# Performance work log

Measured on AMD Instinct MI355X. Metric: run time of the kernel, lower is better.

## Reference

```python
import jax, jax.numpy as jnp
import numpy as np

DEPTH = 6
DIM = 512
HEADS = 8
DH = DIM // HEADS            # 64 head dim
NB = int(DH * np.log(DH))    # 266 FAVOR+ random features (lucidrains default)
FF = 4 * DIM
OUT = 32
B, N = 4, 8192
EPS = 1e-4


def _orthogonal_gaussian(rng, m, d):
    # Blockwise QR orthogonal random matrix with chi-distributed row norms (scaling=0)
    blocks, full = [], m // d
    for _ in range(full):
        q, _ = np.linalg.qr(rng.standard_normal((d, d)))
        blocks.append(q.T)
    rem = m - full * d
    if rem > 0:
        q, _ = np.linalg.qr(rng.standard_normal((d, d)))
        blocks.append(q.T[:rem])
    mat = np.concatenate(blocks, 0)
    mult = np.linalg.norm(rng.standard_normal((m, d)), axis=1)
    return (mult[:, None] * mat).astype(np.float32)


def setup_inputs() -> dict:
    key = jax.random.key(0)
    ks = jax.random.split(key, 16)
    rng = np.random.default_rng(0)
    s = 0.02
    inp = {
        "src": jax.random.normal(ks[0], (B, N, DIM), jnp.float32),
        "proj": jnp.asarray(np.stack([_orthogonal_gaussian(rng, NB, DH) for _ in range(DEPTH)])),
        "ln1_g": jnp.ones((DEPTH, DIM), jnp.float32),
        "ln1_b": jnp.zeros((DEPTH, DIM), jnp.float32),
        "Wq": jax.random.normal(ks[1], (DEPTH, DIM, DIM), jnp.float32) * s,
        "Wk": jax.random.normal(ks[2], (DEPTH, DIM, DIM), jnp.float32) * s,
        "Wv": jax.random.normal(ks[3], (DEPTH, DIM, DIM), jnp.float32) * s,
        "Wo": jax.random.normal(ks[4], (DEPTH, DIM, DIM), jnp.float32) * s,
        "bo": jnp.zeros((DEPTH, DIM), jnp.float32),
        "ln2_g": jnp.ones((DEPTH, DIM), jnp.float32),
        "ln2_b": jnp.zeros((DEPTH, DIM), jnp.float32),
        "W1": jax.random.normal(ks[5], (DEPTH, DIM, FF), jnp.float32) * s,
        "b1": jnp.zeros((DEPTH, FF), jnp.float32),
        "W2": jax.random.normal(ks[6], (DEPTH, FF, DIM), jnp.float32) * s,
        "b2": jnp.zeros((DEPTH, DIM), jnp.float32),
        "fc_w": jax.random.uniform(ks[7], (DIM, OUT), jnp.float32, -0.1, 0.1),
        "fc_b": jnp.zeros((OUT,), jnp.float32),
    }
    return inp


def _layer_norm(x, g, b):
    mu = jnp.mean(x, -1, keepdims=True)
    var = jnp.var(x, -1, keepdims=True)
    return (x - mu) * jax.lax.rsqrt(var + 1e-5) * g + b


def _softmax_kernel(x, proj, is_query):
    # x: [b,h,n,dh], proj: [m,dh] -> positive random features [b,h,n,m]
    dn = DH ** -0.25
    ratio = NB ** -0.5
    xp = jnp.einsum('bhnd,md->bhnm', x * dn, proj)
    diag = (0.5 * jnp.sum(jnp.square(x), -1) * dn * dn)[..., None]
    if is_query:
        mx = jax.lax.stop_gradient(jnp.max(xp, axis=-1, keepdims=True))
    else:
        mx = jax.lax.stop_gradient(jnp.max(xp))
    return ratio * (jnp.exp(xp - diag - mx) + EPS)


def _performer_forward(src, proj, ln1_g, ln1_b, Wq, Wk, Wv, Wo, bo,
                       ln2_g, ln2_b, W1, b1, W2, b2, fc_w, fc_b):
    b, n, _ = src.shape
    x = src
    for i in range(DEPTH):
        h = _layer_norm(x, ln1_g[i], ln1_b[i])
        q = jnp.einsum('bnd,de->bne', h, Wq[i]).reshape(b, n, HEADS, DH).swapaxes(1, 2)
        k = jnp.einsum('bnd,de->bne', h, Wk[i]).reshape(b, n, HEADS, DH).swapaxes(1, 2)
        v = jnp.einsum('bnd,de->bne', h, Wv[i]).reshape(b, n, HEADS, DH).swapaxes(1, 2)
        qp = _softmax_kernel(q, proj[i], True)    # [b,h,n,m]
        kp = _softmax_kernel(k, proj[i], False)
        k_sum = jnp.sum(kp, axis=2)               # [b,h,m]
        d_inv = 1.0 / jnp.einsum('bhnm,bhm->bhn', qp, k_sum)
        ctx = jnp.einsum('bhnm,bhnd->bhmd', kp, v)  # linear-time attention context
        o = jnp.einsum('bhnm,bhmd,bhn->bhnd', qp, ctx, d_inv)
        o = o.swapaxes(1, 2).reshape(b, n, DIM)
        x = x + jnp.einsum('bnd,de->bne', o, Wo[i]) + bo[i]
        h2 = _layer_norm(x, ln2_g[i], ln2_b[i])
        ff = jax.nn.gelu(jnp.einsum('bnd,df->bnf', h2, W1[i]) + b1[i])
        x = x + jnp.einsum('bnf,fd->bnd', ff, W2[i]) + b2[i]
    return jnp.einsum('bnd,do->bno', x, fc_w) + fc_b


def reference(src, proj, ln1_g, ln1_b, Wq, Wk, Wv, Wo, bo,
              ln2_g, ln2_b, W1, b1, W2, b2, fc_w, fc_b):
    return _performer_forward(src, proj, ln1_g, ln1_b, Wq, Wk, Wv, Wo, bo,
                              ln2_g, ln2_b, W1, b1, W2, b2, fc_w, fc_b)
```

## Files before the change

### kernel.cpp

```cpp
#include <hip/hip_runtime.h>
#include <math.h>

#define DIMX 512
#define NHEADS 8
#define DHE 64
#define NB 266
#define MP 288
#define MT 18
#define KPT_LD 136
#define CTXT_LD 296
#define NSTRIP 32
#define FFD 2048
#define OUTD 32
#define SEQ 8192
#define NTOK 32768
#define NLAYER 6
#define PSEQ 16384

#define DN_F 0.35355339059327373f
#define RATIO_F 0.06131393f
#define EPS_F 1e-4f

typedef unsigned short ushort_t;
typedef __attribute__((ext_vector_type(8))) short short8;
typedef __attribute__((ext_vector_type(4))) float floatx4;

__device__ __forceinline__ float tanh_fast(float x) {
    float e = __expf(2.0f * x);
    return 1.0f - 2.0f / (e + 1.0f);
}

__device__ __forceinline__ float gelu_f(float x) {
    float x3 = x * x * x;
    return 0.5f * x * (1.0f + tanh_fast(0.7978845608028654f * (x + 0.044715f * x3)));
}

__device__ __forceinline__ ushort_t f2bf(float f) {
    unsigned int u = __float_as_uint(f);
    unsigned int r = (u + 0x7fffu + ((u >> 16) & 1u)) >> 16;
    return (ushort_t)r;
}

__device__ __forceinline__ float bf2f(ushort_t u) {
    return __uint_as_float(((unsigned int)u) << 16);
}

__device__ __forceinline__ unsigned int fkey(float f) {
    unsigned int u = __float_as_uint(f);
    return (u & 0x80000000u) ? ~u : (u | 0x80000000u);
}
__device__ __forceinline__ float funkey(unsigned int k) {
    unsigned int u = (k & 0x80000000u) ? (k & 0x7fffffffu) : ~k;
    return __uint_as_float(u);
}

__device__ __forceinline__ void gl_lds16(const void* g, void* l) {
    __builtin_amdgcn_global_load_lds(
        (const __attribute__((address_space(1))) unsigned int*)g,
        (__attribute__((address_space(3))) unsigned int*)l, 16, 0, 0);
}

__global__ __launch_bounds__(256) void zero_kernel(float* __restrict__ p, int n) {
    int i = blockIdx.x * 256 + threadIdx.x;
    if (i < n) p[i] = 0.f;
}

__global__ __launch_bounds__(256) void ln_bf16_kernel(const float* __restrict__ x,
                                                      const float* __restrict__ g,
                                                      const float* __restrict__ b,
                                                      ushort_t* __restrict__ out) {
    int row = blockIdx.x * 4 + (threadIdx.x >> 6);
    int lane = threadIdx.x & 63;
    const float4* xr = (const float4*)(x + (size_t)row * DIMX);
    float4 v0 = xr[lane];
    float4 v1 = xr[lane + 64];
    float sum = v0.x + v0.y + v0.z + v0.w + v1.x + v1.y + v1.z + v1.w;
#pragma unroll
    for (int off = 32; off; off >>= 1) sum += __shfl_xor(sum, off);
    float mu = sum * (1.0f / 512.0f);
    float var = (v0.x - mu) * (v0.x - mu) + (v0.y - mu) * (v0.y - mu) +
                (v0.z - mu) * (v0.z - mu) + (v0.w - mu) * (v0.w - mu) +
                (v1.x - mu) * (v1.x - mu) + (v1.y - mu) * (v1.y - mu) +
                (v1.z - mu) * (v1.z - mu) + (v1.w - mu) * (v1.w - mu);
#pragma unroll
    for (int off = 32; off; off >>= 1) var += __shfl_xor(var, off);
    float rstd = rsqrtf(var * (1.0f / 512.0f) + 1e-5f);
    const float4* g4 = (const float4*)g;
    const float4* b4 = (const float4*)b;
    ushort_t* orow = out + (size_t)row * DIMX;
    float4 gg = g4[lane], bb = b4[lane];
    ushort4 o;
    o.x = f2bf((v0.x - mu) * rstd * gg.x + bb.x);
    o.y = f2bf((v0.y - mu) * rstd * gg.y + bb.y);
    o.z = f2bf((v0.z - mu) * rstd * gg.z + bb.z);
    o.w = f2bf((v0.w - mu) * rstd * gg.w + bb.w);
    *(ushort4*)(orow + lane * 4) = o;
    gg = g4[lane + 64]; bb = b4[lane + 64];
    o.x = f2bf((v1.x - mu) * rstd * gg.x + bb.x);
    o.y = f2bf((v1.y - mu) * rstd * gg.y + bb.y);
    o.z = f2bf((v1.z - mu) * rstd * gg.z + bb.z);
    o.w = f2bf((v1.w - mu) * rstd * gg.w + bb.w);
    *(ushort4*)(orow + 256 + lane * 4) = o;
}

__global__ __launch_bounds__(256) void wconv_kernel(const float* __restrict__ W,
                                                    ushort_t* __restrict__ Wt,
                                                    int K, int N) {
    __shared__ float tile[32][33];
    int bx = blockIdx.x * 32;
    int by = blockIdx.y * 32;
    int tx = threadIdx.x & 31, ty = threadIdx.x >> 5;
#pragma unroll
    for (int r = 0; r < 4; r++)
        tile[ty + r * 8][tx] = W[(size_t)(by + ty + r * 8) * N + bx + tx];
    __syncthreads();
#pragma unroll
    for (int r = 0; r < 4; r++)
        Wt[(size_t)(bx + ty + r * 8) * K + by + tx] = f2bf(tile[tx][ty + r * 8]);
}

__global__ __launch_bounds__(256) void wconv4_kernel(const float* __restrict__ W0,
                                                     const float* __restrict__ W1,
                                                     const float* __restrict__ W2,
                                                     const float* __restrict__ W3,
                                                     ushort_t* __restrict__ Wt) {
    __shared__ float tile[32][33];
    const float* Ws[4] = {W0, W1, W2, W3};
    const float* W = Ws[blockIdx.z];
    ushort_t* Wd = Wt + (size_t)blockIdx.z * DIMX * DIMX;
    int bx = blockIdx.x * 32;
    int by = blockIdx.y * 32;
    int tx = threadIdx.x & 31, ty = threadIdx.x >> 5;
#pragma unroll
    for (int r = 0; r < 4; r++)
        tile[ty + r * 8][tx] = W[(size_t)(by + ty + r * 8) * DIMX + bx + tx];
    __syncthreads();
#pragma unroll
    for (int r = 0; r < 4; r++)
        Wd[(size_t)(bx + ty + r * 8) * DIMX + by + tx] = f2bf(tile[tx][ty + r * 8]);
}

__global__ __launch_bounds__(256) void projconv_kernel(const float* __restrict__ proj,
                                                       ushort_t* __restrict__ Pbf) {
    int i = blockIdx.x * 256 + threadIdx.x;
    if (i < MP * DHE) {
        int m = i >> 6;
        Pbf[i] = (m < NB) ? f2bf(proj[i]) : (ushort_t)0;
    }
}

template <int EPI>
__global__ __launch_bounds__(256) void gemm_mfma(const ushort_t* __restrict__ A,
                                                 const ushort_t* __restrict__ Bt,
                                                 const float* __restrict__ bias,
                                                 float* __restrict__ C,
                                                 ushort_t* __restrict__ Cb,
                                                 float* __restrict__ SS,
                                                 int M, int N, int K) {
    __shared__ ushort_t As[128 * 32];
    __shared__ ushort_t Bs[128 * 32];
    int t = threadIdx.x;
    int wave = t >> 6, lane = t & 63;
    int wm = wave >> 1, wn = wave & 1;
    int m0 = blockIdx.x * 128, n0 = blockIdx.y * 128;
    int q = lane >> 4, ml = lane & 15;

    floatx4 acc[4][4];
#pragma unroll
    for (int i = 0; i < 4; i++)
#pragma unroll
        for (int j = 0; j < 4; j++) acc[i][j] = (floatx4)(0.f);

    int srow = (lane >> 2);
    int scol = (lane & 3) * 8;
    const ushort_t* Ag = A + (size_t)(m0 + wave * 32 + srow) * K + scol;
    const ushort_t* Bg = Bt + (size_t)(n0 + wave * 32 + srow) * K + scol;
    ushort_t* AsW = &As[(wave * 32) * 32];
    ushort_t* BsW = &Bs[(wave * 32) * 32];

    for (int k0 = 0; k0 < K; k0 += 32) {
        gl_lds16(Ag + k0, AsW);
        gl_lds16(Ag + k0 + (size_t)16 * K, AsW + 16 * 32);
        gl_lds16(Bg + k0, BsW);
        gl_lds16(Bg + k0 + (size_t)16 * K, BsW + 16 * 32);
        __syncthreads();
        short8 a[4], b[4];
#pragma unroll
        for (int i = 0; i < 4; i++)
            a[i] = *(const short8*)&As[(wm * 64 + i * 16 + ml) * 32 + q * 8];
#pragma unroll
        for (int j = 0; j < 4; j++)
            b[j] = *(const short8*)&Bs[(wn * 64 + j * 16 + ml) * 32 + q * 8];
#pragma unroll
        for (int i = 0; i < 4; i++)
#pragma unroll
            for (int j = 0; j < 4; j++)
                acc[i][j] = __builtin_amdgcn_mfma_f32_16x16x32_bf16(a[i], b[j], acc[i][j], 0, 0, 0);
        __syncthreads();
    }

    if (EPI == 4) {
#pragma unroll
        for (int i = 0; i < 4; i++) {
            size_t r0 = (size_t)m0 + wm * 64 + i * 16 + q * 4;
            int bb = (int)(r0 >> 13);
            int nl = (int)(r0 & (SEQ - 1));
#pragma unroll
            for (int j = 0; j < 4; j++) {
                int col = n0 + wn * 64 + j * 16 + ml;
                int hh = col >> 6, dd = col & 63;
                ushort4 pk;
                pk.x = f2bf(acc[i][j][0]); pk.y = f2bf(acc[i][j][1]);
                pk.z = f2bf(acc[i][j][2]); pk.w = f2bf(acc[i][j][3]);
                *(ushort4*)&Cb[(((size_t)bb * 8 + hh) * DHE + dd) * SEQ + nl] = pk;
            }
        }
    } else if (EPI == 5) {
        int hh = (n0 >> 6) + wn;
#pragma unroll
        for (int i = 0; i < 4; i++) {
#pragma unroll
            for (int r = 0; r < 4; r++) {
                size_t row = (size_t)m0 + wm * 64 + i * 16 + q * 4 + r;
                float sq = 0.f;
#pragma unroll
                for (int j = 0; j < 4; j++) {
                    int col = n0 + wn * 64 + j * 16 + ml;
                    float v = acc[i][j][r];
                    sq += v * v;
                    Cb[row * N + col] = f2bf(v);
                }
                sq += __shfl_xor(sq, 1);
                sq += __shfl_xor(sq, 2);
                sq += __shfl_xor(sq, 4);
                sq += __shfl_xor(sq, 8);
                if (ml == 0) SS[(size_t)hh * PSEQ + row] = sq;
            }
        }
    } else {
#pragma unroll
        for (int i = 0; i < 4; i++) {
#pragma unroll
            for (int r = 0; r < 4; r++) {
                size_t row = (size_t)m0 + wm * 64 + i * 16 + q * 4 + r;
#pragma unroll
                for (int j = 0; j < 4; j++) {
                    int col = n0 + wn * 64 + j * 16 + ml;
                    float v = acc[i][j][r];
                    if (EPI == 1) {
                        C[row * N + col] += v + bias[col];
                    } else if (EPI == 2) {
                        Cb[row * N + col] = f2bf(gelu_f(v + bias[col]));
                    }
                }
            }
        }
    }
}

template <int DOACC, int DOGELU>
__global__ __launch_bounds__(256) void gemm_kernel(const float* __restrict__ A,
                                                   const float* __restrict__ B,
                                                   const float* __restrict__ bias,
                                                   float* __restrict__ C,
                                                   int M, int N, int K) {
    __shared__ float As[16][132];
    __shared__ float Bs[16][132];
    int t = threadIdx.x;
    int tx = t & 15, ty = t >> 4;
    int m0 = blockIdx.x * 128;
    int n0 = blockIdx.y * 128;
    float c[8][8];
#pragma unroll
    for (int i = 0; i < 8; i++)
#pragma unroll
        for (int j = 0; j < 8; j++) c[i][j] = 0.f;
    int am = t >> 1;
    int ak = (t & 1) * 8;
    const float* Aptr = A + (size_t)(m0 + am) * K + ak;
    int bn = (t & 15) * 8;
    int bk = t >> 4;
    bool bvalid = (n0 + bn) < N;
    const float* Bptr = B + (size_t)bk * N + n0 + bn;
    for (int k0 = 0; k0 < K; k0 += 16) {
        float4 a0 = *(const float4*)(Aptr + k0);
        float4 a1 = *(const float4*)(Aptr + k0 + 4);
        As[ak + 0][am] = a0.x; As[ak + 1][am] = a0.y;
        As[ak + 2][am] = a0.z; As[ak + 3][am] = a0.w;
        As[ak + 4][am] = a1.x; As[ak + 5][am] = a1.y;
        As[ak + 6][am] = a1.z; As[ak + 7][am] = a1.w;
        float4 b0 = make_float4(0.f, 0.f, 0.f, 0.f);
        float4 b1v = make_float4(0.f, 0.f, 0.f, 0.f);
        if (bvalid) {
            const float* bp = Bptr + (size_t)k0 * N;
            b0 = *(const float4*)bp;
            b1v = *(const float4*)(bp + 4);
        }
        *(float4*)&Bs[bk][bn] = b0;
        *(float4*)&Bs[bk][bn + 4] = b1v;
        __syncthreads();
#pragma unroll
        for (int kk = 0; kk < 16; kk++) {
            float4 av0 = *(const float4*)&As[kk][ty * 4];
            float4 av1 = *(const float4*)&As[kk][64 + ty * 4];
            float4 bv0 = *(const float4*)&Bs[kk][tx * 4];
            float4 bv1 = *(const float4*)&Bs[kk][64 + tx * 4];
            float a_[8] = {av0.x, av0.y, av0.z, av0.w, av1.x, av1.y, av1.z, av1.w};
            float b_[8] = {bv0.x, bv0.y, bv0.z, bv0.w, bv1.x, bv1.y, bv1.z, bv1.w};
#pragma unroll
            for (int i = 0; i < 8; i++)
#pragma unroll
                for (int j = 0; j < 8; j++) c[i][j] += a_[i] * b_[j];
        }
        __syncthreads();
    }
#pragma unroll
    for (int ih = 0; ih < 2; ih++)
#pragma unroll
        for (int il = 0; il < 4; il++) {
            size_t row = (size_t)m0 + ih * 64 + ty * 4 + il;
#pragma unroll
            for (int jh = 0; jh < 2; jh++) {
                int colbase = n0 + jh * 64 + tx * 4;
                if (colbase < N) {
                    float* cp = C + row * N + colbase;
#pragma unroll
                    for (int jl = 0; jl < 4; jl++) {
                        float v = c[ih * 4 + il][jh * 4 + jl];
                        if (bias) v += bias[colbase + jl];
                        if (DOGELU) v = gelu_f(v);
                        if (DOACC) v += cp[jl];
                        cp[jl] = v;
                    }
                }
            }
        }
}

__global__ __launch_bounds__(512) void kmax_kernel(const ushort_t* __restrict__ Kbf,
                                                   const ushort_t* __restrict__ Pbf,
                                                   unsigned int* __restrict__ kmaxkey) {
    __shared__ float wred[8];
    int tid = threadIdx.x;
    int w = tid >> 6, lane = tid & 63;
    int q = lane >> 4, ml = lane & 15;
    int h = blockIdx.x >> 6, tile = blockIdx.x & 63;
    float lm = -3.0e38f;
#pragma unroll
    for (int sub = 0; sub < 2; sub++) {
        int arow = tile * 256 + sub * 128 + w * 16 + ml;
        short8 af0 = *(const short8*)&Kbf[(size_t)arow * DIMX + h * DHE + q * 8];
        short8 af1 = *(const short8*)&Kbf[(size_t)arow * DIMX + h * DHE + 32 + q * 8];
#pragma unroll
        for (int c = 0; c < 17; c++) {
            floatx4 xp = (floatx4)(0.f);
            short8 b0 = *(const short8*)&Pbf[(c * 16 + ml) * DHE + q * 8];
            short8 b1 = *(const short8*)&Pbf[(c * 16 + ml) * DHE + 32 + q * 8];
            xp = __builtin_amdgcn_mfma_f32_16x16x32_bf16(af0, b0, xp, 0, 0, 0);
            xp = __builtin_amdgcn_mfma_f32_16x16x32_bf16(af1, b1, xp, 0, 0, 0);
            if (c * 16 + ml < NB)
                lm = fmaxf(lm, fmaxf(fmaxf(xp[0], xp[1]), fmaxf(xp[2], xp[3])));
        }
    }
    lm *= DN_F;
#pragma unroll
    for (int off = 32; off; off >>= 1) lm = fmaxf(lm, __shfl_xor(lm, off));
    if (lane == 0) wred[w] = lm;
    __syncthreads();
    if (tid == 0) {
        float bm = wred[0];
#pragma unroll
        for (int ww = 1; ww < 8; ww++) bm = fmaxf(bm, wred[ww]);
        atomicMax(kmaxkey, fkey(bm));
    }
}

__global__ __launch_bounds__(512, 4) void kctx_kernel(const ushort_t* __restrict__ Kbf,
                                                      const ushort_t* __restrict__ Pbf,
                                                      const float* __restrict__ SS,
                                                      const unsigned int* __restrict__ kmaxkey,
                                                      const ushort_t* __restrict__ Vt,
                                                      float* __restrict__ CTXP,
                                                      float* __restrict__ KSUM) {
    __shared__ ushort_t kpT[144 * KPT_LD];
    __shared__ float ksum_l[MP];
    int tid = threadIdx.x;
    int w = tid >> 6, lane = tid & 63;
    int q = lane >> 4, ml = lane & 15;
    int bh = blockIdx.x >> 5, s = blockIdx.x & 31;
    int b = bh >> 3, h = bh & 7;
    float mx = funkey(*kmaxkey);
    if (tid < MP) ksum_l[tid] = 0.f;
    __syncthreads();
    floatx4 ctxa[2][5];
#pragma unroll
    for (int hf = 0; hf < 2; hf++)
#pragma unroll
        for (int i = 0; i < 5; i++) ctxa[hf][i] = (floatx4)(0.f);

#pragma unroll
    for (int sub = 0; sub < 2; sub++) {
        int tb = b * SEQ + s * 256 + sub * 128;
        int arow = tb + w * 16 + ml;
        short8 af0 = *(const short8*)&Kbf[(size_t)arow * DIMX + h * DHE + q * 8];
        short8 af1 = *(const short8*)&Kbf[(size_t)arow * DIMX + h * DHE + 32 + q * 8];
        float ssr[4];
#pragma unroll
        for (int r = 0; r < 4; r++) ssr[r] = SS[h * PSEQ + tb + w * 16 + q * 4 + r];
#pragma unroll
        for (int hf = 0; hf < 2; hf++) {
#pragma unroll
            for (int cl = 0; cl < 9; cl++) {
                int c = hf * 9 + cl;
                floatx4 xp = (floatx4)(0.f);
                short8 b0 = *(const short8*)&Pbf[(c * 16 + ml) * DHE + q * 8];
                short8 b1 = *(const short8*)&Pbf[(c * 16 + ml) * DHE + 32 + q * 8];
                xp = __builtin_amdgcn_mfma_f32_16x16x32_bf16(af0, b0, xp, 0, 0, 0);
                xp = __builtin_amdgcn_mfma_f32_16x16x32_bf16(af1, b1, xp, 0, 0, 0);
                int m = c * 16 + ml;
                bool val = m < NB;
                float kpv[4];
#pragma unroll
                for (int r = 0; r < 4; r++)
                    kpv[r] = val ? RATIO_F * (__expf(xp[r] * DN_F - ssr[r] * 0.0625f - mx) + EPS_F)
                                 : 0.f;
                ushort4 pk;
                pk.x = f2bf(kpv[0]); pk.y = f2bf(kpv[1]);
                pk.z = f2bf(kpv[2]); pk.w = f2bf(kpv[3]);
                *(ushort4*)&kpT[(cl * 16 + ml) * KPT_LD + w * 16 + q * 4] = pk;
                float s4 = kpv[0] + kpv[1] + kpv[2] + kpv[3];
                s4 += __shfl_xor(s4, 16);
                s4 += __shfl_xor(s4, 32);
                if (q == 0) atomicAdd(&ksum_l[m], s4);
            }
            __syncthreads();
#pragma unroll
            for (int sk = 0; sk < 4; sk++) {
#pragma unroll
                for (int i = 0; i < 5; i++) {
                    if (i < 4 || w < 4) {
                        int tt = w + i * 8;
                        int mtl = tt >> 2, dt = tt & 3;
                        short8 a = *(const short8*)&kpT[(mtl * 16 + ml) * KPT_LD + sk * 32 + q * 8];
                        short8 bv = *(const short8*)&Vt[((size_t)bh * DHE + dt * 16 + ml) * SEQ +
                                                        s * 256 + sub * 128 + sk * 32 + q * 8];
                        ctxa[hf][i] = __builtin_amdgcn_mfma_f32_16x16x32_bf16(a, bv, ctxa[hf][i], 0, 0, 0);
                    }
                }
            }
            __syncthreads();
        }
    }
    float* stg = (float*)kpT;
    float* cp = CTXP + ((size_t)bh * NSTRIP + s) * (MP * DHE);
#pragma unroll
    for (int hf = 0; hf < 2; hf++) {
        __syncthreads();
#pragma unroll
        for (int i = 0; i < 5; i++) {
            if (i < 4 || w < 4) {
                int tt = w + i * 8;
                int mtl = tt >> 2, dt = tt & 3;
#pragma unroll
                for (int r = 0; r < 4; r++)
                    stg[(mtl * 16 + q * 4 + r) * 68 + dt * 16 + ml] = ctxa[hf][i][r];
            }
        }
        __syncthreads();
        float4* cp4 = (float4*)(cp + (size_t)hf * 144 * DHE);
        for (int e4 = tid; e4 < 2304; e4 += 512) {
            int row = e4 >> 4, col4 = e4 & 15;
            cp4[e4] = ((const float4*)stg)[row * 17 + col4];
        }
    }
    if (tid < MP) atomicAdd(&KSUM[bh * MP + tid], ksum_l[tid]);
}

__global__ __launch_bounds__(256) void ctx_reduce_kernel(const float* __restrict__ CTXP,
                                                         ushort_t* __restrict__ CTXbf) {
    int i = blockIdx.x * 256 + threadIdx.x;
    if (i < 16 * MP * DHE) {
        int bh = i / (MP * DHE);
        int e = i - bh * (MP * DHE);
        float s = 0.f;
#pragma unroll
        for (int st = 0; st < NSTRIP; st++)
            s += CTXP[((size_t)bh * NSTRIP + st) * (MP * DHE) + e];
        int m = e >> 6, d = e & 63;
        CTXbf[((size_t)bh * DHE + d) * CTXT_LD + m] = f2bf(s);
    }
}

__global__ __launch_bounds__(256, 3) void qo_kernel(const ushort_t* __restrict__ Qbf,
                                                    const ushort_t* __restrict__ Pbf,
                                                    const float* __restrict__ SS,
                                                    const ushort_t* __restrict__ CTXbf,
                                                    const float* __restrict__ KSUM,
                                                    ushort_t* __restrict__ Ob) {
    __shared__ ushort_t ctxt[DHE * CTXT_LD];
    __shared__ ushort_t qpA[4][16][40];
    __shared__ float ksl[MP];
    int tid = threadIdx.x;
    int w = tid >> 6, lane = tid & 63;
    int q = lane >> 4, ml = lane & 15;
    int bh = blockIdx.x >> 7, tile = blockIdx.x & 127;
    int b = bh >> 3, h = bh & 7;
    const short8* Cg8 = (const short8*)(CTXbf + (size_t)bh * (DHE * CTXT_LD));
    short8* ct8 = (short8*)ctxt;
    for (int e = tid; e < (DHE * CTXT_LD) / 8; e += 256)
        ct8[e] = Cg8[e];
    ksl[tid] = KSUM[bh * MP + tid];
    if (tid < MP - 256) ksl[256 + tid] = KSUM[bh * MP + 256 + tid];
    __syncthreads();
    int nl = tile * 64 + w * 16;
    int arow = b * SEQ + nl + ml;
    short8 af0 = *(const short8*)&Qbf[(size_t)arow * DIMX + h * DHE + q * 8];
    short8 af1 = *(const short8*)&Qbf[(size_t)arow * DIMX + h * DHE + 32 + q * 8];
    floatx4 xp[MT];
#pragma unroll
    for (int c = 0; c < MT; c++) {
        xp[c] = (floatx4)(0.f);
        short8 b0 = *(const short8*)&Pbf[(c * 16 + ml) * DHE + q * 8];
        short8 b1 = *(const short8*)&Pbf[(c * 16 + ml) * DHE + 32 + q * 8];
        xp[c] = __builtin_amdgcn_mfma_f32_16x16x32_bf16(af0, b0, xp[c], 0, 0, 0);
        xp[c] = __builtin_amdgcn_mfma_f32_16x16x32_bf16(af1, b1, xp[c], 0, 0, 0);
    }
    float ssr[4], rm[4], dp[4], dinv[4];
#pragma unroll
    for (int r = 0; r < 4; r++) {
        ssr[r] = SS[h * PSEQ + b * SEQ + nl + q * 4 + r];
        rm[r] = -3.0e38f;
        dp[r] = 0.f;
    }
#pragma unroll
    for (int c = 0; c < MT; c++) {
        int m = c * 16 + ml;
        bool val = m < NB;
#pragma unroll
        for (int r = 0; r < 4; r++) {
            float tv = xp[c][r] * DN_F;
            xp[c][r] = tv;
            if (val) rm[r] = fmaxf(rm[r], tv);
        }
    }
#pragma unroll
    for (int r = 0; r < 4; r++) {
        rm[r] = fmaxf(rm[r], __shfl_xor(rm[r], 1));
        rm[r] = fmaxf(rm[r], __shfl_xor(rm[r], 2));
        rm[r] = fmaxf(rm[r], __shfl_xor(rm[r], 4));
        rm[r] = fmaxf(rm[r], __shfl_xor(rm[r], 8));
    }
#pragma unroll
    for (int c = 0; c < MT; c++) {
        int m = c * 16 + ml;
        bool val = m < NB;
        float km = ksl[m];
#pragma unroll
        for (int r = 0; r < 4; r++) {
            float v = val ? RATIO_F * (__expf(xp[c][r] - ssr[r] * 0.0625f - rm[r]) + EPS_F) : 0.f;
            xp[c][r] = v;
            dp[r] += v * km;
        }
    }
#pragma unroll
    for (int r = 0; r < 4; r++) {
        dp[r] += __shfl_xor(dp[r], 1);
        dp[r] += __shfl_xor(dp[r], 2);
        dp[r] += __shfl_xor(dp[r], 4);
        dp[r] += __shfl_xor(dp[r], 8);
        dinv[r] = 1.0f / dp[r];
    }
    floatx4 oacc[4];
#pragma unroll
    for (int dt = 0; dt < 4; dt++) oacc[dt] = (floatx4)(0.f);
#pragma unroll
    for (int ks = 0; ks < 9; ks++) {
#pragma unroll
        for (int cc = 0; cc < 2; cc++) {
            int c = 2 * ks + cc;
#pragma unroll
            for (int r = 0; r < 4; r++)
                qpA[w][q * 4 + r][cc * 16 + ml] = f2bf(xp[c][r]);
        }
        short8 a = *(const short8*)&qpA[w][ml][q * 8];
#pragma unroll
        for (int dt = 0; dt < 4; dt++) {
            short8 bv = *(const short8*)&ctxt[(dt * 16 + ml) * CTXT_LD + ks * 32 + q * 8];
            oacc[dt] = __builtin_amdgcn_mfma_f32_16x16x32_bf16(a, bv, oacc[dt], 0, 0, 0);
        }
    }
#pragma unroll
    for (int dt = 0; dt < 4; dt++)
#pragma unroll
        for (int r = 0; r < 4; r++)
            Ob[(size_t)(b * SEQ + nl + q * 4 + r) * DIMX + h * DHE + dt * 16 + ml] =
                f2bf(oacc[dt][r] * dinv[r]);
}

extern "C" void kernel_launch(void* const* d_in, const int* in_sizes, int n_in,
                              void* d_out, int out_size, void* d_ws, size_t ws_size,
                              hipStream_t stream) {
    (void)in_sizes; (void)n_in; (void)out_size; (void)ws_size;
    const float* src  = (const float*)d_in[0];
    const float* proj = (const float*)d_in[1];
    const float* ln1g = (const float*)d_in[2];
    const float* ln1b = (const float*)d_in[3];
    const float* Wq   = (const float*)d_in[4];
    const float* Wk   = (const float*)d_in[5];
    const float* Wv   = (const float*)d_in[6];
    const float* Wo   = (const float*)d_in[7];
    const float* bo   = (const float*)d_in[8];
    const float* ln2g = (const float*)d_in[9];
    const float* ln2b = (const float*)d_in[10];
    const float* W1   = (const float*)d_in[11];
    const float* b1   = (const float*)d_in[12];
    const float* W2   = (const float*)d_in[13];
    const float* b2   = (const float*)d_in[14];
    const float* fcw  = (const float*)d_in[15];
    const float* fcb  = (const float*)d_in[16];
    float* out = (float*)d_out;

    const size_t TD   = (size_t)NTOK * DIMX;
    const size_t PD   = (size_t)PSEQ * DIMX;
    float*    X    = (float*)d_ws;
    ushort_t* Hs   = (ushort_t*)(X + TD);
    ushort_t* KQbf = Hs + PD;
    ushort_t* Vt   = KQbf + PD;
    float*    CTXP = (float*)(Vt + PD);
    ushort_t* Obuf = (ushort_t*)CTXP;
    ushort_t* CTXbf = (ushort_t*)(CTXP + (size_t)16 * NSTRIP * MP * DHE);
    float*    KSUM = (float*)(CTXbf + (size_t)16 * DHE * CTXT_LD);
    unsigned int* KMAX = (unsigned int*)(KSUM + 16 * MP);
    float*    SS   = (float*)(KMAX + 4);
    ushort_t* Pbf  = (ushort_t*)(SS + (size_t)NHEADS * PSEQ);
    ushort_t* Wtb  = Pbf + MP * DHE;
    ushort_t* Wqt = Wtb;
    ushort_t* Wkt = Wqt + DIMX * DIMX;
    ushort_t* Wvt = Wkt + DIMX * DIMX;
    ushort_t* Wot = Wvt + DIMX * DIMX;
    ushort_t* W1t = Wot + DIMX * DIMX;
    ushort_t* W2t = W1t + (size_t)DIMX * FFD;
    ushort_t* Hid = KQbf;

    hipMemcpyAsync(X, src, sizeof(float) * TD, hipMemcpyDeviceToDevice, stream);

    dim3 gP(PSEQ / 128, DIMX / 128);
    dim3 gF1(PSEQ / 128, FFD / 128);
    const int lnGrid = PSEQ / 4;
    for (int L = 0; L < NLAYER; L++) {
        const float* pj = proj + (size_t)L * NB * DHE;
        wconv4_kernel<<<dim3(16, 16, 4), 256, 0, stream>>>(
            Wq + (size_t)L * DIMX * DIMX, Wk + (size_t)L * DIMX * DIMX,
            Wv + (size_t)L * DIMX * DIMX, Wo + (size_t)L * DIMX * DIMX, Wqt);
        wconv_kernel<<<dim3(64, 16), 256, 0, stream>>>(W1 + (size_t)L * DIMX * FFD, W1t, DIMX, FFD);
        wconv_kernel<<<dim3(16, 64), 256, 0, stream>>>(W2 + (size_t)L * FFD * DIMX, W2t, FFD, DIMX);
        projconv_kernel<<<(MP * DHE + 255) / 256, 256, 0, stream>>>(pj, Pbf);
        zero_kernel<<<1, 256, 0, stream>>>((float*)KMAX, 1);
        for (int p = 0; p < 2; p++) {
            const float* Xp = X + (size_t)p * PD;
            ln_bf16_kernel<<<lnGrid, 256, 0, stream>>>(Xp, ln1g + L * DIMX, ln1b + L * DIMX, Hs);
            gemm_mfma<5><<<gP, 256, 0, stream>>>(Hs, Wkt, nullptr, nullptr, KQbf, SS, PSEQ, DIMX, DIMX);
            kmax_kernel<<<512, 512, 0, stream>>>(KQbf, Pbf, KMAX);
        }
        for (int pp = 0; pp < 2; pp++) {
            int p = 1 - pp;
            float* Xp = X + (size_t)p * PD;
            if (p == 0) {
                ln_bf16_kernel<<<lnGrid, 256, 0, stream>>>(Xp, ln1g + L * DIMX, ln1b + L * DIMX, Hs);
                gemm_mfma<5><<<gP, 256, 0, stream>>>(Hs, Wkt, nullptr, nullptr, KQbf, SS, PSEQ, DIMX, DIMX);
            }
            gemm_mfma<4><<<gP, 256, 0, stream>>>(Hs, Wvt, nullptr, nullptr, Vt, nullptr, PSEQ, DIMX, DIMX);
            zero_kernel<<<(16 * MP + 255) / 256, 256, 0, stream>>>(KSUM, 16 * MP);
            kctx_kernel<<<16 * NSTRIP, 512, 0, stream>>>(KQbf, Pbf, SS, KMAX, Vt, CTXP, KSUM);
            ctx_reduce_kernel<<<(16 * MP * DHE + 255) / 256, 256, 0, stream>>>(CTXP, CTXbf);
            gemm_mfma<5><<<gP, 256, 0, stream>>>(Hs, Wqt, nullptr, nullptr, KQbf, SS, PSEQ, DIMX, DIMX);
            qo_kernel<<<2048, 256, 0, stream>>>(KQbf, Pbf, SS, CTXbf, KSUM, Obuf);
            gemm_mfma<1><<<gP, 256, 0, stream>>>(Obuf, Wot, bo + L * DIMX, Xp, nullptr, nullptr, PSEQ, DIMX, DIMX);
            ln_bf16_kernel<<<lnGrid, 256, 0, stream>>>(Xp, ln2g + L * DIMX, ln2b + L * DIMX, Hs);
            gemm_mfma<2><<<gF1, 256, 0, stream>>>(Hs, W1t, b1 + L * FFD, nullptr, Hid, nullptr, PSEQ, FFD, DIMX);
            gemm_mfma<1><<<gP, 256, 0, stream>>>(Hid, W2t, b2 + L * DIMX, Xp, nullptr, nullptr, PSEQ, DIMX, FFD);
        }
    }
    gemm_kernel<0, 0><<<dim3(NTOK / 128, 1), 256, 0, stream>>>(X, fcw, fcb, out, NTOK, OUTD, DIMX);
}
```

Baseline: 5.488 ms.

## Double-buffer GEMM LDS tiles, swizzle block order, simplify GELU

The MFMA GEMM now uses two LDS buffers, so global-to-LDS loads for the next K-slice are issued while the current slice is being multiplied, removing one barrier per iteration. Block indices are remapped with an XCD-style swizzle (groups of 8) to improve L2 locality across chiplets. GELU is rewritten in the equivalent sigmoid form with a hardware reciprocal, which cuts ALU work in the FFN epilogue. Double-buffering doubles LDS use per block, which may lower occupancy, and the swizzle assumes the total block count is divisible by 8.

```diff
diff --git a/kernel.cpp b/kernel.cpp
--- a/kernel.cpp
+++ b/kernel.cpp
@@ -25,14 +25,12 @@
 typedef __attribute__((ext_vector_type(8))) short short8;
 typedef __attribute__((ext_vector_type(4))) float floatx4;
 
-__device__ __forceinline__ float tanh_fast(float x) {
-    float e = __expf(2.0f * x);
-    return 1.0f - 2.0f / (e + 1.0f);
-}
-
 __device__ __forceinline__ float gelu_f(float x) {
-    float x3 = x * x * x;
-    return 0.5f * x * (1.0f + tanh_fast(0.7978845608028654f * (x + 0.044715f * x3)));
+    float s = x * x;
+    float t = fmaf(0.044715f, s, 1.0f);
+    float u = -1.5957691216057308f * x * t;
+    float e = __expf(u);
+    return x * __builtin_amdgcn_rcpf(1.0f + e);
 }
 
 __device__ __forceinline__ ushort_t f2bf(float f) {
@@ -157,12 +155,16 @@
                                                  ushort_t* __restrict__ Cb,
                                                  float* __restrict__ SS,
                                                  int M, int N, int K) {
-    __shared__ ushort_t As[128 * 32];
-    __shared__ ushort_t Bs[128 * 32];
+    __shared__ ushort_t As[2][128 * 32];
+    __shared__ ushort_t Bs[2][128 * 32];
     int t = threadIdx.x;
     int wave = t >> 6, lane = t & 63;
     int wm = wave >> 1, wn = wave & 1;
-    int m0 = blockIdx.x * 128, n0 = blockIdx.y * 128;
+    int gy = gridDim.y;
+    int orig = blockIdx.x + blockIdx.y * gridDim.x;
+    int cpx = (gridDim.x * gy) >> 3;
+    int swz = (orig & 7) * cpx + (orig >> 3);
+    int m0 = (swz / gy) * 128, n0 = (swz - (swz / gy) * gy) * 128;
     int q = lane >> 4, ml = lane & 15;
 
     floatx4 acc[4][4];
@@ -175,28 +177,54 @@
     int scol = (lane & 3) * 8;
     const ushort_t* Ag = A + (size_t)(m0 + wave * 32 + srow) * K + scol;
     const ushort_t* Bg = Bt + (size_t)(n0 + wave * 32 + srow) * K + scol;
-    ushort_t* AsW = &As[(wave * 32) * 32];
-    ushort_t* BsW = &Bs[(wave * 32) * 32];
-
-    for (int k0 = 0; k0 < K; k0 += 32) {
-        gl_lds16(Ag + k0, AsW);
-        gl_lds16(Ag + k0 + (size_t)16 * K, AsW + 16 * 32);
-        gl_lds16(Bg + k0, BsW);
-        gl_lds16(Bg + k0 + (size_t)16 * K, BsW + 16 * 32);
-        __syncthreads();
+    ushort_t* AsW[2] = {&As[0][(wave * 32) * 32], &As[1][(wave * 32) * 32]};
+    ushort_t* BsW[2] = {&Bs[0][(wave * 32) * 32], &Bs[1][(wave * 32) * 32]};
+
+    gl_lds16(Ag, AsW[0]);
+    gl_lds16(Ag + (size_t)16 * K, AsW[0] + 16 * 32);
+    gl_lds16(Bg, BsW[0]);
+    gl_lds16(Bg + (size_t)16 * K, BsW[0] + 16 * 32);
+    __syncthreads();
+
+    int cur = 0;
+    for (int k0 = 32; k0 < K; k0 += 32) {
+        int nxt = cur ^ 1;
+        gl_lds16(Ag + k0, AsW[nxt]);
+        gl_lds16(Ag + k0 + (size_t)16 * K, AsW[nxt] + 16 * 32);
+        gl_lds16(Bg + k0, BsW[nxt]);
+        gl_lds16(Bg + k0 + (size_t)16 * K, BsW[nxt] + 16 * 32);
+        const ushort_t* Ac = &As[cur][0];
+        const ushort_t* Bc = &Bs[cur][0];
         short8 a[4], b[4];
 #pragma unroll
         for (int i = 0; i < 4; i++)
-            a[i] = *(const short8*)&As[(wm * 64 + i * 16 + ml) * 32 + q * 8];
+            a[i] = *(const short8*)&Ac[(wm * 64 + i * 16 + ml) * 32 + q * 8];
 #pragma unroll
         for (int j = 0; j < 4; j++)
-            b[j] = *(const short8*)&Bs[(wn * 64 + j * 16 + ml) * 32 + q * 8];
+            b[j] = *(const short8*)&Bc[(wn * 64 + j * 16 + ml) * 32 + q * 8];
 #pragma unroll
         for (int i = 0; i < 4; i++)
 #pragma unroll
             for (int j = 0; j < 4; j++)
                 acc[i][j] = __builtin_amdgcn_mfma_f32_16x16x32_bf16(a[i], b[j], acc[i][j], 0, 0, 0);
         __syncthreads();
+        cur = nxt;
+    }
+    {
+        const ushort_t* Ac = &As[cur][0];
+        const ushort_t* Bc = &Bs[cur][0];
+        short8 a[4], b[4];
+#pragma unroll
+        for (int i = 0; i < 4; i++)
+            a[i] = *(const short8*)&Ac[(wm * 64 + i * 16 + ml) * 32 + q * 8];
+#pragma unroll
+        for (int j = 0; j < 4; j++)
+            b[j] = *(const short8*)&Bc[(wn * 64 + j * 16 + ml) * 32 + q * 8];
+#pragma unroll
+        for (int i = 0; i < 4; i++)
+#pragma unroll
+            for (int j = 0; j < 4; j++)
+                acc[i][j] = __builtin_amdgcn_mfma_f32_16x16x32_bf16(a[i], b[j], acc[i][j], 0, 0, 0);
     }
 
     if (EPI == 4) {
```

Result: faster. 4.986 ms (-9.2%).
